# Optimization experiments

Measured on AMD Instinct MI355X. Metric: run time of the kernel, lower is better.

Reference implementation:

```python
import jax, jax.numpy as jnp
import numpy as np

B, N, D_IN, D_OUT = 2, 4096, 768, 768


def setup_inputs() -> dict:
    key = jax.random.key(0)
    kx, kq, kk, kv = jax.random.split(key, 4)
    x = jax.random.normal(kx, (B, N, D_IN), dtype=jnp.float32)
    # Linear(d_in, d_out, bias=False) weights, stored as [d_in, d_out]
    scale = 1.0 / np.sqrt(D_IN)
    Wq = jax.random.normal(kq, (D_IN, D_OUT), dtype=jnp.float32) * scale
    Wk = jax.random.normal(kk, (D_IN, D_OUT), dtype=jnp.float32) * scale
    Wv = jax.random.normal(kv, (D_IN, D_OUT), dtype=jnp.float32) * scale
    return {"x": x, "Wq": Wq, "Wk": Wk, "Wv": Wv}


def reference(x, Wq, Wk, Wv):
    # q,k,v: [B, N, D_OUT]
    q = jnp.einsum('bnd,de->bne', x, Wq)
    k = jnp.einsum('bnd,de->bne', x, Wk)
    v = jnp.einsum('bnd,de->bne', x, Wv)
    # Full [B, N, N] score matrix (naive attention, as in source).
    # NOTE: source's masked_fill is non-in-place and discarded, so NO causal
    # mask is actually applied -- reproduced faithfully here.
    scores = jnp.einsum('bqe,bke->bqk', q, k) / jnp.sqrt(jnp.float32(k.shape[-1]))
    weights = jax.nn.softmax(scores, axis=-1)
    # dropout rate 0.0 / eval mode -> identity
    out = jnp.einsum('bqk,bke->bqe', weights, v)  # [B, N, D_OUT]
    return out
```

## Files before the change

kernel.cpp:

```cpp
#include <hip/hip_runtime.h>

typedef __bf16 bf16x8 __attribute__((ext_vector_type(8)));
typedef float f32x4 __attribute__((ext_vector_type(4)));
typedef unsigned short us8 __attribute__((ext_vector_type(8)));

#define GAS __attribute__((address_space(1)))
#define LAS __attribute__((address_space(3)))

__device__ __forceinline__ unsigned short f32_to_bf16(float f) {
    unsigned int u = __float_as_uint(f);
    u += 0x7FFFu + ((u >> 16) & 1u);
    return (unsigned short)(u >> 16);
}

__device__ __forceinline__ float bf16_to_f32(unsigned short h) {
    return __uint_as_float((unsigned int)h << 16);
}

__device__ __forceinline__ void load16(const unsigned short* g, unsigned short* l) {
    __builtin_amdgcn_global_load_lds((GAS unsigned int*)g, (LAS unsigned int*)l, 16, 0, 0);
}

__global__ __launch_bounds__(1024) void prep(
    const float* __restrict__ x, unsigned short* __restrict__ Xbf,
    const float* __restrict__ W0, const float* __restrict__ W1, const float* __restrict__ W2,
    unsigned short* __restrict__ T0, unsigned short* __restrict__ T1, unsigned short* __restrict__ T2)
{
    __shared__ float tile[32][33];
    const int id = blockIdx.x;
    const int t = threadIdx.x;
    if (id < 1536) {
        int i = id * 1024 + t;
        float4 v = ((const float4*)x)[i];
        ushort4 o;
        o.x = f32_to_bf16(v.x); o.y = f32_to_bf16(v.y);
        o.z = f32_to_bf16(v.z); o.w = f32_to_bf16(v.w);
        ((ushort4*)Xbf)[i] = o;
    } else {
        const int tid = id - 1536;
        const int z = tid / 576, rem = tid % 576;
        const int by = rem / 24, bx = rem % 24;
        const float* W = (z == 0) ? W0 : (z == 1) ? W1 : W2;
        unsigned short* T = (z == 0) ? T0 : (z == 1) ? T1 : T2;
        const int r0 = by * 32, c0 = bx * 32;
        const int tx = t & 31, ty = t >> 5;
        tile[ty][tx] = W[(size_t)(r0 + ty) * 768 + c0 + tx];
        __syncthreads();
        T[(size_t)(c0 + ty) * 768 + r0 + tx] = f32_to_bf16(tile[tx][ty]);
    }
}

template <typename CT>
__global__ __launch_bounds__(256) void gemm_nt(
    const unsigned short* __restrict__ A, const unsigned short* __restrict__ B,
    CT* __restrict__ C, int K, int lda, int ldb, int ldc,
    size_t sA, size_t sB, size_t sC, float alpha)
{
    A += (size_t)blockIdx.z * sA;
    B += (size_t)blockIdx.z * sB;
    C += (size_t)blockIdx.z * sC;
    const int m0 = blockIdx.y * 128;
    const int n0 = blockIdx.x * 128;
    const int t = threadIdx.x;
    const int lane = t & 63;
    const int w = t >> 6;
    const int wm = (w >> 1) * 64;
    const int wn = (w & 1) * 64;

    __shared__ unsigned short At[128 * 64];
    __shared__ unsigned short Bt[128 * 64];

    f32x4 acc[4][4];
#pragma unroll
    for (int i = 0; i < 4; ++i)
#pragma unroll
        for (int j = 0; j < 4; ++j) acc[i][j] = (f32x4){0.f, 0.f, 0.f, 0.f};

    const int r15 = lane & 15;
    const int qa = lane >> 4;

    for (int k0 = 0; k0 < K; k0 += 64) {
#pragma unroll
        for (int i = 0; i < 4; ++i) {
            const int c = i * 256 + t;
            const int row = c >> 3;
            const int cc = (c & 7) ^ (row & 7);
            load16(A + (size_t)(m0 + row) * lda + k0 + cc * 8, &At[c * 8]);
            load16(B + (size_t)(n0 + row) * ldb + k0 + cc * 8, &Bt[c * 8]);
        }
        __syncthreads();

#pragma unroll
        for (int ks = 0; ks < 2; ++ks) {
            bf16x8 af[4], bf[4];
#pragma unroll
            for (int mi = 0; mi < 4; ++mi) {
                const int row = wm + mi * 16 + r15;
                af[mi] = *(const bf16x8*)&At[row * 64 + (((ks << 2) + qa) ^ (row & 7)) * 8];
            }
#pragma unroll
            for (int ni = 0; ni < 4; ++ni) {
                const int row = wn + ni * 16 + r15;
                bf[ni] = *(const bf16x8*)&Bt[row * 64 + (((ks << 2) + qa) ^ (row & 7)) * 8];
            }
#pragma unroll
            for (int mi = 0; mi < 4; ++mi)
#pragma unroll
                for (int ni = 0; ni < 4; ++ni)
                    acc[mi][ni] = __builtin_amdgcn_mfma_f32_16x16x32_bf16(
                        af[mi], bf[ni], acc[mi][ni], 0, 0, 0);
        }
        __syncthreads();
    }

    const int cr = (lane >> 4) * 4;
#pragma unroll
    for (int mi = 0; mi < 4; ++mi) {
#pragma unroll
        for (int ni = 0; ni < 4; ++ni) {
            const int gm = m0 + wm + mi * 16 + cr;
            const int gn = n0 + wn + ni * 16 + r15;
#pragma unroll
            for (int r = 0; r < 4; ++r) {
                float v = alpha * acc[mi][ni][r];
                if constexpr (sizeof(CT) == 2)
                    C[(size_t)(gm + r) * ldc + gn] = (CT)f32_to_bf16(v);
                else
                    C[(size_t)(gm + r) * ldc + gn] = v;
            }
        }
    }
}

__global__ __launch_bounds__(256) void gemm_s_exp(
    const unsigned short* __restrict__ Q, const unsigned short* __restrict__ Kb,
    unsigned short* __restrict__ Sexp, float alpha)
{
    const unsigned short* A = Q + (size_t)blockIdx.z * 3145728;
    const unsigned short* B = Kb + (size_t)blockIdx.z * 3145728;
    unsigned short* C = Sexp + (size_t)blockIdx.z * 16777216;
    const int lda = 768, ldb = 768, ldc = 4096;
    const int m0 = blockIdx.y * 128;
    const int n0 = blockIdx.x * 128;
    const int t = threadIdx.x;
    const int lane = t & 63;
    const int w = t >> 6;
    const int wm = (w >> 1) * 64;
    const int wn = (w & 1) * 64;

    __shared__ unsigned short At[128 * 64];
    __shared__ unsigned short Bt[128 * 64];

    f32x4 acc[4][4];
#pragma unroll
    for (int i = 0; i < 4; ++i)
#pragma unroll
        for (int j = 0; j < 4; ++j) acc[i][j] = (f32x4){0.f, 0.f, 0.f, 0.f};

    const int r15 = lane & 15;
    const int qa = lane >> 4;

    for (int k0 = 0; k0 < 768; k0 += 64) {
#pragma unroll
        for (int i = 0; i < 4; ++i) {
            const int c = i * 256 + t;
            const int row = c >> 3;
            const int cc = (c & 7) ^ (row & 7);
            load16(A + (size_t)(m0 + row) * lda + k0 + cc * 8, &At[c * 8]);
            load16(B + (size_t)(n0 + row) * ldb + k0 + cc * 8, &Bt[c * 8]);
        }
        __syncthreads();

#pragma unroll
        for (int ks = 0; ks < 2; ++ks) {
            bf16x8 af[4], bf[4];
#pragma unroll
            for (int mi = 0; mi < 4; ++mi) {
                const int row = wm + mi * 16 + r15;
                af[mi] = *(const bf16x8*)&At[row * 64 + (((ks << 2) + qa) ^ (row & 7)) * 8];
            }
#pragma unroll
            for (int ni = 0; ni < 4; ++ni) {
                const int row = wn + ni * 16 + r15;
                bf[ni] = *(const bf16x8*)&Bt[row * 64 + (((ks << 2) + qa) ^ (row & 7)) * 8];
            }
#pragma unroll
            for (int mi = 0; mi < 4; ++mi)
#pragma unroll
                for (int ni = 0; ni < 4; ++ni)
                    acc[mi][ni] = __builtin_amdgcn_mfma_f32_16x16x32_bf16(
                        af[mi], bf[ni], acc[mi][ni], 0, 0, 0);
        }
        __syncthreads();
    }

    const int cr = (lane >> 4) * 4;
#pragma unroll
    for (int mi = 0; mi < 4; ++mi)
#pragma unroll
        for (int ni = 0; ni < 4; ++ni) {
            const int gm = m0 + wm + mi * 16 + cr;
            const int gn = n0 + wn + ni * 16 + r15;
#pragma unroll
            for (int r = 0; r < 4; ++r)
                C[(size_t)(gm + r) * ldc + gn] = f32_to_bf16(__expf(alpha * acc[mi][ni][r]));
        }
}

__global__ __launch_bounds__(256) void gemm_nt_splitk(
    const unsigned short* __restrict__ P, const unsigned short* __restrict__ Vt,
    unsigned short* __restrict__ Part)
{
    const int f = blockIdx.x;
    const int r8 = f & 7;
    const int tq = f >> 3;
    const int n  = tq % 6;
    const int v  = tq / 6;
    const int u  = v * 8 + r8;
    const int batch = u & 1;
    const int split = (u >> 1) & 3;
    const int m = u >> 3;

    const unsigned short* A = P + (size_t)batch * 16777216 + (size_t)split * 1024;
    const unsigned short* B = Vt + (size_t)batch * 4096 + (size_t)split * 1024;
    unsigned short* C = Part + (size_t)(split * 2 + batch) * 3145728;
    const int lda = 4096, ldb = 8192, ldc = 768;
    const int m0 = m * 128;
    const int n0 = n * 128;
    const int t = threadIdx.x;
    const int lane = t & 63;
    const int w = t >> 6;
    const int wm = (w >> 1) * 64;
    const int wn = (w & 1) * 64;

    __shared__ unsigned short At[128 * 64];
    __shared__ unsigned short Bt[128 * 64];

    f32x4 acc[4][4];
#pragma unroll
    for (int i = 0; i < 4; ++i)
#pragma unroll
        for (int j = 0; j < 4; ++j) acc[i][j] = (f32x4){0.f, 0.f, 0.f, 0.f};

    const int r15 = lane & 15;
    const int qa = lane >> 4;

    for (int k0 = 0; k0 < 1024; k0 += 64) {
#pragma unroll
        for (int i = 0; i < 4; ++i) {
            const int c = i * 256 + t;
            const int row = c >> 3;
            const int cc = (c & 7) ^ (row & 7);
            load16(A + (size_t)(m0 + row) * lda + k0 + cc * 8, &At[c * 8]);
            load16(B + (size_t)(n0 + row) * ldb + k0 + cc * 8, &Bt[c * 8]);
        }
        __syncthreads();

#pragma unroll
        for (int ks = 0; ks < 2; ++ks) {
            bf16x8 af[4], bf[4];
#pragma unroll
            for (int mi = 0; mi < 4; ++mi) {
                const int row = wm + mi * 16 + r15;
                af[mi] = *(const bf16x8*)&At[row * 64 + (((ks << 2) + qa) ^ (row & 7)) * 8];
            }
#pragma unroll
            for (int ni = 0; ni < 4; ++ni) {
                const int row = wn + ni * 16 + r15;
                bf[ni] = *(const bf16x8*)&Bt[row * 64 + (((ks << 2) + qa) ^ (row & 7)) * 8];
            }
#pragma unroll
            for (int mi = 0; mi < 4; ++mi)
#pragma unroll
                for (int ni = 0; ni < 4; ++ni)
                    acc[mi][ni] = __builtin_amdgcn_mfma_f32_16x16x32_bf16(
                        af[mi], bf[ni], acc[mi][ni], 0, 0, 0);
        }
        __syncthreads();
    }

    const int cr = (lane >> 4) * 4;
#pragma unroll
    for (int mi = 0; mi < 4; ++mi) {
#pragma unroll
        for (int ni = 0; ni < 4; ++ni) {
            const int gm = m0 + wm + mi * 16 + cr;
            const int gn = n0 + wn + ni * 16 + r15;
#pragma unroll
            for (int r = 0; r < 4; ++r)
                C[(size_t)(gm + r) * ldc + gn] = f32_to_bf16(acc[mi][ni][r]);
        }
    }
}

__global__ __launch_bounds__(256) void reduce_norm_rows(
    const unsigned short* __restrict__ Sexp, const unsigned short* __restrict__ Part,
    float* __restrict__ out)
{
    const int g = blockIdx.x;
    const int batch = g >> 12;
    const int r = g & 4095;
    const int t = threadIdx.x;
    const int wv = t >> 6, ln = t & 63;

    const unsigned short* srow = Sexp + (size_t)batch * 16777216 + (size_t)r * 4096;
    us8 a = ((const us8*)srow)[t];
    us8 b = ((const us8*)srow)[t + 256];
    float s = 0.f;
#pragma unroll
    for (int j = 0; j < 8; ++j) s += bf16_to_f32(a[j]) + bf16_to_f32(b[j]);
#pragma unroll
    for (int off = 32; off > 0; off >>= 1) s += __shfl_down(s, off, 64);
    __shared__ float red[4];
    if (ln == 0) red[wv] = s;
    __syncthreads();
    const float inv = 1.f / (red[0] + red[1] + red[2] + red[3]);

    if (t < 192) {
        const int c = t * 4;
        float4 acc = {0.f, 0.f, 0.f, 0.f};
#pragma unroll
        for (int sgroup = 0; sgroup < 4; ++sgroup) {
            const unsigned short* p = Part
                + ((size_t)(sgroup * 2 + batch) * 4096 + r) * 768 + c;
            ushort4 u = *(const ushort4*)p;
            acc.x += bf16_to_f32(u.x);
            acc.y += bf16_to_f32(u.y);
            acc.z += bf16_to_f32(u.z);
            acc.w += bf16_to_f32(u.w);
        }
        float4 o;
        o.x = acc.x * inv; o.y = acc.y * inv; o.z = acc.z * inv; o.w = acc.w * inv;
        *(float4*)(out + (size_t)g * 768 + c) = o;
    }
}

extern "C" void kernel_launch(void* const* d_in, const int* in_sizes, int n_in,
                              void* d_out, int out_size, void* d_ws, size_t ws_size,
                              hipStream_t stream) {
    const float* x  = (const float*)d_in[0];
    const float* Wq = (const float*)d_in[1];
    const float* Wk = (const float*)d_in[2];
    const float* Wv = (const float*)d_in[3];
    float* out = (float*)d_out;

    char* base = (char*)d_ws;
    size_t off = 0;
    auto alloc = [&](size_t b) { char* p = base + off; off += (b + 255) & ~(size_t)255; return p; };

    unsigned short* Xbf = (unsigned short*)alloc(8192ull * 768 * 2);
    unsigned short* WqT = (unsigned short*)alloc(768ull * 768 * 2);
    unsigned short* WkT = (unsigned short*)alloc(768ull * 768 * 2);
    unsigned short* WvT = (unsigned short*)alloc(768ull * 768 * 2);
    unsigned short* Qb  = (unsigned short*)alloc(8192ull * 768 * 2);
    unsigned short* Kb  = (unsigned short*)alloc(8192ull * 768 * 2);
    unsigned short* Vt  = (unsigned short*)alloc(768ull * 8192 * 2);
    unsigned short* Sexp = (unsigned short*)alloc(2ull * 4096 * 4096 * 2);
    unsigned short* Part = (unsigned short*)alloc(8ull * 3145728 * 2);
    (void)ws_size; (void)in_sizes; (void)n_in; (void)out_size; (void)WkT;

    prep<<<dim3(3264), dim3(1024), 0, stream>>>(x, Xbf, Wq, Wk, Wv, WqT, WkT, WvT);
    gemm_nt<unsigned short><<<dim3(6, 64, 2), dim3(256), 0, stream>>>(
        Xbf, WqT, Qb, 768, 768, 768, 768,
         0,  589824,  6291456, 1.0f);
    gemm_nt<unsigned short><<<dim3(64, 6, 1), dim3(256), 0, stream>>>(
        WvT, Xbf, Vt, 768, 768, 768, 8192, 0, 0, 0, 1.0f);
    gemm_s_exp<<<dim3(32, 32, 2), dim3(256), 0, stream>>>(
        Qb, Kb, Sexp, 0.03608439182435161f);
    gemm_nt_splitk<<<dim3(1536), dim3(256), 0, stream>>>(Sexp, Vt, Part);
    reduce_norm_rows<<<dim3(8192), dim3(256), 0, stream>>>(Sexp, Part, out);
}
```

Before: 277.0 us.

## Use 256x256 double-buffered LDS GEMM core for score and PV kernels

Replaces the 128x128 single-buffer score-exp and split-K PV GEMMs with a shared 256x256-tile core that uses 512 threads and 8 waves. It double-buffers LDS so global-to-LDS loads for the next K tile overlap the MFMA work, and raises wave priority around the MFMA blocks. Larger tiles raise arithmetic intensity and cut LDS reloads. The cost is 128KB of LDS per block and a high register count, which limits occupancy. The PV grid also loses the swizzled block ordering used for L2 locality.

```diff
diff --git a/kernel.cpp b/kernel.cpp
--- a/kernel.cpp
+++ b/kernel.cpp
@@ -132,165 +132,161 @@
     }
 }
 
-__global__ __launch_bounds__(256) void gemm_s_exp(
+template <int NT, bool EXP>
+__device__ __forceinline__ void gemm256_core(
+    const unsigned short* __restrict__ A, const unsigned short* __restrict__ B,
+    unsigned short* __restrict__ C,
+    int m0, int n0, int lda, int ldb, int ldc, float alpha)
+{
+    __shared__ unsigned short As[2][256 * 64];
+    __shared__ unsigned short Bs[2][256 * 64];
+
+    const int t = threadIdx.x;
+    const int lane = t & 63;
+    const int w = t >> 6;
+    const int wm = (w >> 2) * 128;
+    const int wn = (w & 3) * 64;
+    const int r15 = lane & 15;
+    const int qa = lane >> 4;
+
+    const unsigned short* srcA[4];
+    const unsigned short* srcB[4];
+    int dstOff[4];
+#pragma unroll
+    for (int i = 0; i < 4; ++i) {
+        const int c = i * 512 + t;
+        const int row = c >> 3;
+        const int cc = (c & 7) ^ (row & 7);
+        srcA[i] = A + (size_t)(m0 + row) * lda + cc * 8;
+        srcB[i] = B + (size_t)(n0 + row) * ldb + cc * 8;
+        dstOff[i] = c * 8;
+    }
+
+    auto stageA = [&](int b, int kbase) {
+#pragma unroll
+        for (int i = 0; i < 4; ++i)
+            load16(srcA[i] + kbase, &As[b][dstOff[i]]);
+    };
+    auto stageB = [&](int b, int kbase) {
+#pragma unroll
+        for (int i = 0; i < 4; ++i)
+            load16(srcB[i] + kbase, &Bs[b][dstOff[i]]);
+    };
+
+    stageA(0, 0);
+    stageB(0, 0);
+
+    int offA[8][2], offB[4][2];
+#pragma unroll
+    for (int mi = 0; mi < 8; ++mi) {
+        const int row = wm + mi * 16 + r15;
+#pragma unroll
+        for (int ks = 0; ks < 2; ++ks)
+            offA[mi][ks] = row * 64 + (((ks << 2) + qa) ^ (row & 7)) * 8;
+    }
+#pragma unroll
+    for (int ni = 0; ni < 4; ++ni) {
+        const int row = wn + ni * 16 + r15;
+#pragma unroll
+        for (int ks = 0; ks < 2; ++ks)
+            offB[ni][ks] = row * 64 + (((ks << 2) + qa) ^ (row & 7)) * 8;
+    }
+
+    f32x4 acc[8][4];
+#pragma unroll
+    for (int i = 0; i < 8; ++i)
+#pragma unroll
+        for (int j = 0; j < 4; ++j) acc[i][j] = (f32x4){0.f, 0.f, 0.f, 0.f};
+
+    for (int tt = 0; tt < NT; ++tt) {
+        const int b = tt & 1;
+        const bool st = (tt + 1) < NT;
+        const int kn = (tt + 1) << 6;
+
+        asm volatile("s_waitcnt vmcnt(0)" ::: "memory");
+        __builtin_amdgcn_s_barrier();
+        asm volatile("" ::: "memory");
+
+#pragma unroll
+        for (int ks = 0; ks < 2; ++ks) {
+#pragma unroll
+            for (int mh = 0; mh < 2; ++mh) {
+                bf16x8 bf[4];
+                if (mh == 0) {
+#pragma unroll
+                    for (int ni = 0; ni < 4; ++ni)
+                        bf[ni] = *(const bf16x8*)&Bs[b][offB[ni][ks]];
+                } else {
+#pragma unroll
+                    for (int ni = 0; ni < 4; ++ni)
+                        bf[ni] = *(const bf16x8*)&Bs[b][offB[ni][ks]];
+                }
+                bf16x8 af[4];
+#pragma unroll
+                for (int i = 0; i < 4; ++i)
+                    af[i] = *(const bf16x8*)&As[b][offA[mh * 4 + i][ks]];
+
+                if (ks == 0 && st) {
+                    if (mh == 0) stageA(b ^ 1, kn);
+                    else         stageB(b ^ 1, kn);
+                }
+
+                __builtin_amdgcn_s_barrier();
+                asm volatile("s_waitcnt lgkmcnt(0)" ::: "memory");
+                __builtin_amdgcn_sched_barrier(0);
+                __builtin_amdgcn_s_setprio(1);
+#pragma unroll
+                for (int i = 0; i < 4; ++i)
+#pragma unroll
+                    for (int ni = 0; ni < 4; ++ni)
+                        acc[mh * 4 + i][ni] = __builtin_amdgcn_mfma_f32_16x16x32_bf16(
+                            af[i], bf[ni], acc[mh * 4 + i][ni], 0, 0, 0);
+                __builtin_amdgcn_s_setprio(0);
+                __builtin_amdgcn_s_barrier();
+            }
+        }
+    }
+
+    const int cr = (lane >> 4) * 4;
+#pragma unroll
+    for (int mi = 0; mi < 8; ++mi) {
+#pragma unroll
+        for (int ni = 0; ni < 4; ++ni) {
+            const int gm = m0 + wm + mi * 16 + cr;
+            const int gn = n0 + wn + ni * 16 + r15;
+#pragma unroll
+            for (int r = 0; r < 4; ++r) {
+                float v = alpha * acc[mi][ni][r];
+                if constexpr (EXP) v = __expf(v);
+                C[(size_t)(gm + r) * ldc + gn] = f32_to_bf16(v);
+            }
+        }
+    }
+}
+
+__global__ __launch_bounds__(512, 2) void gemm_s_exp2(
     const unsigned short* __restrict__ Q, const unsigned short* __restrict__ Kb,
     unsigned short* __restrict__ Sexp, float alpha)
 {
     const unsigned short* A = Q + (size_t)blockIdx.z * 3145728;
     const unsigned short* B = Kb + (size_t)blockIdx.z * 3145728;
     unsigned short* C = Sexp + (size_t)blockIdx.z * 16777216;
-    const int lda = 768, ldb = 768, ldc = 4096;
-    const int m0 = blockIdx.y * 128;
-    const int n0 = blockIdx.x * 128;
-    const int t = threadIdx.x;
-    const int lane = t & 63;
-    const int w = t >> 6;
-    const int wm = (w >> 1) * 64;
-    const int wn = (w & 1) * 64;
-
-    __shared__ unsigned short At[128 * 64];
-    __shared__ unsigned short Bt[128 * 64];
-
-    f32x4 acc[4][4];
-#pragma unroll
-    for (int i = 0; i < 4; ++i)
-#pragma unroll
-        for (int j = 0; j < 4; ++j) acc[i][j] = (f32x4){0.f, 0.f, 0.f, 0.f};
-
-    const int r15 = lane & 15;
-    const int qa = lane >> 4;
-
-    for (int k0 = 0; k0 < 768; k0 += 64) {
-#pragma unroll
-        for (int i = 0; i < 4; ++i) {
-            const int c = i * 256 + t;
-            const int row = c >> 3;
-            const int cc = (c & 7) ^ (row & 7);
-            load16(A + (size_t)(m0 + row) * lda + k0 + cc * 8, &At[c * 8]);
-            load16(B + (size_t)(n0 + row) * ldb + k0 + cc * 8, &Bt[c * 8]);
-        }
-        __syncthreads();
-
-#pragma unroll
-        for (int ks = 0; ks < 2; ++ks) {
-            bf16x8 af[4], bf[4];
-#pragma unroll
-            for (int mi = 0; mi < 4; ++mi) {
-                const int row = wm + mi * 16 + r15;
-                af[mi] = *(const bf16x8*)&At[row * 64 + (((ks << 2) + qa) ^ (row & 7)) * 8];
-            }
-#pragma unroll
-            for (int ni = 0; ni < 4; ++ni) {
-                const int row = wn + ni * 16 + r15;
-                bf[ni] = *(const bf16x8*)&Bt[row * 64 + (((ks << 2) + qa) ^ (row & 7)) * 8];
-            }
-#pragma unroll
-            for (int mi = 0; mi < 4; ++mi)
-#pragma unroll
-                for (int ni = 0; ni < 4; ++ni)
-                    acc[mi][ni] = __builtin_amdgcn_mfma_f32_16x16x32_bf16(
-                        af[mi], bf[ni], acc[mi][ni], 0, 0, 0);
-        }
-        __syncthreads();
-    }
-
-    const int cr = (lane >> 4) * 4;
-#pragma unroll
-    for (int mi = 0; mi < 4; ++mi)
-#pragma unroll
-        for (int ni = 0; ni < 4; ++ni) {
-            const int gm = m0 + wm + mi * 16 + cr;
-            const int gn = n0 + wn + ni * 16 + r15;
-#pragma unroll
-            for (int r = 0; r < 4; ++r)
-                C[(size_t)(gm + r) * ldc + gn] = f32_to_bf16(__expf(alpha * acc[mi][ni][r]));
-        }
-}
-
-__global__ __launch_bounds__(256) void gemm_nt_splitk(
+    gemm256_core<12, true>(A, B, C, blockIdx.y * 256, blockIdx.x * 256,
+                           768, 768, 4096, alpha);
+}
+
+__global__ __launch_bounds__(512, 2) void gemm_splitk2(
     const unsigned short* __restrict__ P, const unsigned short* __restrict__ Vt,
     unsigned short* __restrict__ Part)
 {
-    const int f = blockIdx.x;
-    const int r8 = f & 7;
-    const int tq = f >> 3;
-    const int n  = tq % 6;
-    const int v  = tq / 6;
-    const int u  = v * 8 + r8;
-    const int batch = u & 1;
-    const int split = (u >> 1) & 3;
-    const int m = u >> 3;
-
+    const int z = blockIdx.z;
+    const int batch = z & 1;
+    const int split = z >> 1;
     const unsigned short* A = P + (size_t)batch * 16777216 + (size_t)split * 1024;
     const unsigned short* B = Vt + (size_t)batch * 4096 + (size_t)split * 1024;
-    unsigned short* C = Part + (size_t)(split * 2 + batch) * 3145728;
-    const int lda = 4096, ldb = 8192, ldc = 768;
-    const int m0 = m * 128;
-    const int n0 = n * 128;
-    const int t = threadIdx.x;
-    const int lane = t & 63;
-    const int w = t >> 6;
-    const int wm = (w >> 1) * 64;
-    const int wn = (w & 1) * 64;
-
-    __shared__ unsigned short At[128 * 64];
-    __shared__ unsigned short Bt[128 * 64];
-
-    f32x4 acc[4][4];
-#pragma unroll
-    for (int i = 0; i < 4; ++i)
-#pragma unroll
-        for (int j = 0; j < 4; ++j) acc[i][j] = (f32x4){0.f, 0.f, 0.f, 0.f};
-
-    const int r15 = lane & 15;
-    const int qa = lane >> 4;
-
-    for (int k0 = 0; k0 < 1024; k0 += 64) {
-#pragma unroll
-        for (int i = 0; i < 4; ++i) {
-            const int c = i * 256 + t;
-            const int row = c >> 3;
-            const int cc = (c & 7) ^ (row & 7);
-            load16(A + (size_t)(m0 + row) * lda + k0 + cc * 8, &At[c * 8]);
-            load16(B + (size_t)(n0 + row) * ldb + k0 + cc * 8, &Bt[c * 8]);
-        }
-        __syncthreads();
-
-#pragma unroll
-        for (int ks = 0; ks < 2; ++ks) {
-            bf16x8 af[4], bf[4];
-#pragma unroll
-            for (int mi = 0; mi < 4; ++mi) {
-                const int row = wm + mi * 16 + r15;
-                af[mi] = *(const bf16x8*)&At[row * 64 + (((ks << 2) + qa) ^ (row & 7)) * 8];
-            }
-#pragma unroll
-            for (int ni = 0; ni < 4; ++ni) {
-                const int row = wn + ni * 16 + r15;
-                bf[ni] = *(const bf16x8*)&Bt[row * 64 + (((ks << 2) + qa) ^ (row & 7)) * 8];
-            }
-#pragma unroll
-            for (int mi = 0; mi < 4; ++mi)
-#pragma unroll
-                for (int ni = 0; ni < 4; ++ni)
-                    acc[mi][ni] = __builtin_amdgcn_mfma_f32_16x16x32_bf16(
-                        af[mi], bf[ni], acc[mi][ni], 0, 0, 0);
-        }
-        __syncthreads();
-    }
-
-    const int cr = (lane >> 4) * 4;
-#pragma unroll
-    for (int mi = 0; mi < 4; ++mi) {
-#pragma unroll
-        for (int ni = 0; ni < 4; ++ni) {
-            const int gm = m0 + wm + mi * 16 + cr;
-            const int gn = n0 + wn + ni * 16 + r15;
-#pragma unroll
-            for (int r = 0; r < 4; ++r)
-                C[(size_t)(gm + r) * ldc + gn] = f32_to_bf16(acc[mi][ni][r]);
-        }
-    }
+    unsigned short* C = Part + (size_t)z * 3145728;
+    gemm256_core<16, false>(A, B, C, blockIdx.y * 256, blockIdx.x * 256,
+                            4096, 8192, 768, 1.0f);
 }
 
 __global__ __launch_bounds__(256) void reduce_norm_rows(
@@ -365,8 +361,8 @@
          0,  589824,  6291456, 1.0f);
     gemm_nt<unsigned short><<<dim3(64, 6, 1), dim3(256), 0, stream>>>(
         WvT, Xbf, Vt, 768, 768, 768, 8192, 0, 0, 0, 1.0f);
-    gemm_s_exp<<<dim3(32, 32, 2), dim3(256), 0, stream>>>(
+    gemm_s_exp2<<<dim3(16, 16, 2), dim3(512), 0, stream>>>(
         Qb, Kb, Sexp, 0.03608439182435161f);
-    gemm_nt_splitk<<<dim3(1536), dim3(256), 0, stream>>>(Sexp, Vt, Part);
+    gemm_splitk2<<<dim3(3, 16, 8), dim3(512), 0, stream>>>(Sexp, Vt, Part);
     reduce_norm_rows<<<dim3(8192), dim3(256), 0, stream>>>(Sexp, Part, out);
 }
```

After: 305.4 us. 10.3% more time.
